# Performance work log

Measured on AMD Instinct MI355X. Metric: run time of the kernel, lower is better.

The kernel has to match this reference:

```python
import jax, jax.numpy as jnp
import numpy as np

EMBED_DIM = 1024
NUM_HEADS = 16


def setup_inputs() -> dict:
    key = jax.random.key(0)
    k_x, k_qw, k_qb, k_pw, k_bias, k_mask = jax.random.split(key, 6)
    B, N, C = 2, 2048, EMBED_DIM
    x = jax.random.normal(k_x, (B, N, C), dtype=jnp.float32)
    # torch Linear params: weight (out,in), bias (out,)
    qkv_w = jax.random.normal(k_qw, (3 * C, C), dtype=jnp.float32) * (C ** -0.5)
    qkv_b = jax.random.normal(k_qb, (3 * C,), dtype=jnp.float32) * 0.02
    proj_w = jax.random.normal(k_pw, (C, C), dtype=jnp.float32) * (C ** -0.5)
    proj_b = jnp.zeros((C,), dtype=jnp.float32)
    # nn.Parameter(torch.zeros(H,1,1)); small noise so the bias is non-trivial
    physics_bias = jax.random.normal(k_bias, (NUM_HEADS, 1, 1), dtype=jnp.float32) * 0.01
    physics_mask = jax.random.randint(k_mask, (B, 1, N, N), 0, 2).astype(jnp.int32)
    return {"x": x, "qkv_w": qkv_w, "qkv_b": qkv_b, "proj_w": proj_w,
            "proj_b": proj_b, "physics_bias": physics_bias,
            "physics_mask": physics_mask}


def reference(x, qkv_w, qkv_b, proj_w, proj_b, physics_bias, physics_mask):
    B, N, C = x.shape
    H = NUM_HEADS
    Dh = C // H
    # fused QKV projection: (B,N,3C) -> (B,N,3,H,Dh)
    qkv = (x @ qkv_w.T + qkv_b).reshape(B, N, 3, H, Dh)
    q = jnp.transpose(qkv[:, :, 0], (0, 2, 1, 3))  # (B,H,N,Dh)
    k = jnp.transpose(qkv[:, :, 1], (0, 2, 1, 3))
    v = jnp.transpose(qkv[:, :, 2], (0, 2, 1, 3))
    scale = Dh ** -0.5
    attn = jnp.einsum('bhnd,bhmd->bhnm', q, k) * scale  # (B,H,N,N)
    attn = attn + physics_bias  # (H,1,1) broadcasts per head
    attn = jnp.where(physics_mask == 0, -jnp.inf, attn)
    attn = jax.nn.softmax(attn, axis=-1)
    out = jnp.einsum('bhnm,bhmd->bhnd', attn, v)  # (B,H,N,Dh)
    out = jnp.transpose(out, (0, 2, 1, 3)).reshape(B, N, C)
    return out @ proj_w.T + proj_b
```

## Files before the change

### kernel.cpp

```cpp
#include <hip/hip_runtime.h>
#include <hip/hip_bf16.h>
#include <stdint.h>
#include <math.h>


typedef __bf16 bf16;
typedef __bf16 bf16x8 __attribute__((ext_vector_type(8)));
typedef __bf16 bf16x4 __attribute__((ext_vector_type(4)));
typedef float f32x4 __attribute__((ext_vector_type(4)));
typedef float f32x16 __attribute__((ext_vector_type(16)));

#define MFMA(a,b,c) __builtin_amdgcn_mfma_f32_16x16x32_bf16((a),(b),(c),0,0,0)
#define MFMA32(a,b,c) __builtin_amdgcn_mfma_f32_32x32x16_bf16((a),(b),(c),0,0,0)
#define L2E 1.44269504f

#if __has_builtin(__builtin_amdgcn_exp2f)
#define EXP2(x) __builtin_amdgcn_exp2f(x)
#else
#define EXP2(x) exp2f(x)
#endif

#if __has_builtin(__builtin_amdgcn_sbfe)
#define SBFE1(x,o) __builtin_amdgcn_sbfe((int)(x), (int)(o), 1)
#else
#define SBFE1(x,o) (((int)(((unsigned)(x)) << (31 - (o)))) >> 31)
#endif

__device__ __forceinline__ void async16(const void* g, void* l) {
  __builtin_amdgcn_global_load_lds(
      (const __attribute__((address_space(1))) void*)g,
      (__attribute__((address_space(3))) void*)l, 16, 0, 0);
}

__device__ __forceinline__ unsigned cvt_pk_bf16(float a, float b) {
  unsigned r;
  asm("v_cvt_pk_bf16_f32 %0, %1, %2" : "=v"(r) : "v"(a), "v"(b));
  return r;
}

__device__ __forceinline__ float maskf(float p, unsigned m, int pos) {
  int sm = SBFE1(m, pos);
  return __uint_as_float(__float_as_uint(p) & (unsigned)sm);
}

__device__ __forceinline__ void lane32_swap(unsigned a, unsigned b,
                                            unsigned& x, unsigned& y, int hi) {
#if __has_builtin(__builtin_amdgcn_permlane32_swap)
  auto r = __builtin_amdgcn_permlane32_swap((int)a, (int)b, false, false);
  x = (unsigned)r[0];
  y = (unsigned)r[1];
#else
  unsigned pa_ = __shfl_xor(a, 32), pb_ = __shfl_xor(b, 32);
  x = hi ? pb_ : a;
  y = hi ? b : pa_;
#endif
}

template <bool F32>
__device__ __forceinline__ bf16x8 ld8(const void* base, size_t off) {
  if constexpr (F32) {
    const float* p = (const float*)base + off;
    float4 u = *(const float4*)p;
    float4 v = *(const float4*)(p + 4);
    bf16x8 r;
    r[0] = (bf16)u.x; r[1] = (bf16)u.y; r[2] = (bf16)u.z; r[3] = (bf16)u.w;
    r[4] = (bf16)v.x; r[5] = (bf16)v.y; r[6] = (bf16)v.z; r[7] = (bf16)v.w;
    return r;
  } else {
    return *(const bf16x8*)((const bf16*)base + off);
  }
}

__global__ __launch_bounds__(256) void prep(const int* __restrict__ mask,
                                            unsigned long long* __restrict__ mbg,
                                            const float* __restrict__ x, bf16* __restrict__ xb,
                                            const float* __restrict__ qw, bf16* __restrict__ qwb,
                                            const float* __restrict__ pw, bf16* __restrict__ pwb) {
  int bid = blockIdx.x, tid = threadIdx.x;
  if (bid < 4096) {
    int lane = tid & 63, wv = tid >> 6;
    const int* mrow = mask + (size_t)bid * 2048;
#pragma unroll
    for (int i = 0; i < 8; ++i) {
      int w = wv * 8 + i;
      unsigned long long bal = __ballot(mrow[w * 64 + lane] != 0);
      if (lane == 0) mbg[(size_t)bid * 32 + w] = bal;
    }
  } else if (bid < 6144) {
    size_t i = ((size_t)(bid - 4096) * 256 + tid) * 8;
    *(bf16x8*)&xb[i] = ld8<true>(x, i);
  } else if (bid < 7680) {
    size_t i = ((size_t)(bid - 6144) * 256 + tid) * 8;
    *(bf16x8*)&qwb[i] = ld8<true>(qw, i);
  } else {
    size_t i = ((size_t)(bid - 7680) * 256 + tid) * 8;
    *(bf16x8*)&pwb[i] = ld8<true>(pw, i);
  }
}

template <int BROWS>
__device__ __forceinline__ void gemm_pipe(const bf16* __restrict__ A,
                                          const bf16* __restrict__ B,
                                          int m0, int n0,
                                          f32x4 acc[4][BROWS / 32],
                                          char* sm) {
  const int ABYTES = 128 * 128;
  const int BUF = ABYTES + BROWS * 128;
  int tid = threadIdx.x, lane = tid & 63, wv = tid >> 6;
  int wm = wv & 1, wn = wv >> 1, g = lane >> 4, li = lane & 15;
  int ln8 = lane >> 3;
  int scol = ((lane & 7) << 4) ^ ((ln8 & 7) << 4);

  const char* Ab = (const char*)A;
  const char* Bb = (const char*)B;

#pragma unroll
  for (int c = 0; c < 4; ++c) {
    int r = wv * 32 + c * 8;
    async16(Ab + (size_t)(m0 + r + ln8) * 2048 + scol, sm + r * 128);
  }
#pragma unroll
  for (int c = 0; c < BROWS / 32; ++c) {
    int r = wv * (BROWS / 4) + c * 8;
    async16(Bb + (size_t)(n0 + r + ln8) * 2048 + scol, sm + ABYTES + r * 128);
  }

  int kt2 = 128;
  for (int p = 0; p < 16; ++p) {
    asm volatile("s_waitcnt vmcnt(0)" ::: "memory");
    __builtin_amdgcn_s_barrier();
    __builtin_amdgcn_sched_barrier(0);
    if (p < 15) {
      char* bas = sm + ((p + 1) & 1) * BUF;
#pragma unroll
      for (int c = 0; c < 4; ++c) {
        int r = wv * 32 + c * 8;
        async16(Ab + (size_t)(m0 + r + ln8) * 2048 + kt2 + scol, bas + r * 128);
      }
#pragma unroll
      for (int c = 0; c < BROWS / 32; ++c) {
        int r = wv * (BROWS / 4) + c * 8;
        async16(Bb + (size_t)(n0 + r + ln8) * 2048 + kt2 + scol,
                bas + ABYTES + r * 128);
      }
      kt2 += 128;
    }
    __builtin_amdgcn_sched_barrier(0);
    const char* basA = sm + (p & 1) * BUF;
    const char* basB = basA + ABYTES;
#pragma unroll
    for (int ks = 0; ks < 2; ++ks) {
      bf16x8 af[4], bg[BROWS / 32];
#pragma unroll
      for (int i = 0; i < 4; ++i) {
        int row = wm * 64 + i * 16 + li;
        af[i] = *(const bf16x8*)(basA + row * 128 +
                                 ((ks * 64 + g * 16) ^ ((row & 7) << 4)));
      }
#pragma unroll
      for (int j = 0; j < BROWS / 32; ++j) {
        int row = wn * (BROWS / 2) + j * 16 + li;
        bg[j] = *(const bf16x8*)(basB + row * 128 +
                                 ((ks * 64 + g * 16) ^ ((row & 7) << 4)));
      }
#pragma unroll
      for (int i = 0; i < 4; ++i)
#pragma unroll
        for (int j = 0; j < BROWS / 32; ++j)
          acc[i][j] = MFMA(af[i], bg[j], acc[i][j]);
    }
  }
}

template <bool AF32, bool BF32>
__device__ __forceinline__ void gemm_core(const void* __restrict__ A,
                                          const void* __restrict__ B,
                                          int m0, int n0,
                                          f32x4 acc[4][4],
                                          bf16* Al, bf16* Bl) {
  const int K = 1024;
  int tid = threadIdx.x, lane = tid & 63, wv = tid >> 6;
  int wm = wv & 1, wn = wv >> 1, g = lane >> 4, li = lane & 15;
  int r8 = lane >> 3, c8 = lane & 7;

  for (int kt = 0; kt < K; kt += 64) {
    bf16x8 ta[4], tb[4];
#pragma unroll
    for (int i2 = 0; i2 < 4; ++i2) {
      int row = wv * 32 + i2 * 8 + r8;
      ta[i2] = ld8<AF32>(A, (size_t)(m0 + row) * K + kt + c8 * 8);
      tb[i2] = ld8<BF32>(B, (size_t)(n0 + row) * K + kt + c8 * 8);
    }
    __syncthreads();
#pragma unroll
    for (int i2 = 0; i2 < 4; ++i2) {
      int row = wv * 32 + i2 * 8 + r8;
      *(bf16x8*)&Al[row * 64 + c8 * 8] = ta[i2];
      *(bf16x8*)&Bl[row * 64 + c8 * 8] = tb[i2];
    }
    __syncthreads();
#pragma unroll
    for (int ks = 0; ks < 64; ks += 32) {
      bf16x8 af[4], bg[4];
#pragma unroll
      for (int i = 0; i < 4; ++i)
        af[i] = *(const bf16x8*)&Al[(wm * 64 + i * 16 + li) * 64 + ks + g * 8];
#pragma unroll
      for (int j = 0; j < 4; ++j)
        bg[j] = *(const bf16x8*)&Bl[(wn * 64 + j * 16 + li) * 64 + ks + g * 8];
#pragma unroll
      for (int i = 0; i < 4; ++i)
#pragma unroll
        for (int j = 0; j < 4; ++j)
          acc[i][j] = MFMA(af[i], bg[j], acc[i][j]);
    }
  }
}

__device__ __forceinline__ void epi_qk(f32x4 acc[4][4], int m0, int n0,
                                       const float* __restrict__ bias,
                                       bf16* __restrict__ qg, bf16* __restrict__ kg) {
  int lane = threadIdx.x & 63, wv = threadIdx.x >> 6;
  int wm = wv & 1, wn = wv >> 1, g = lane >> 4, li = lane & 15;
#pragma unroll
  for (int i = 0; i < 4; ++i) {
    int o = m0 + wm * 64 + i * 16 + g * 4;
    int s = o >> 10, h = (o >> 6) & 15, d = o & 63;
    float sc = s ? 1.0f : 0.125f * L2E;
    float b0 = bias[o], b1 = bias[o + 1], b2 = bias[o + 2], b3 = bias[o + 3];
    bf16* dstb = s ? kg : qg;
#pragma unroll
    for (int j = 0; j < 4; ++j) {
      int t = n0 + wn * 64 + j * 16 + li;
      int b = t >> 11, n = t & 2047;
      ushort4 pk;
      ((bf16*)&pk)[0] = (bf16)((acc[i][j][0] + b0) * sc);
      ((bf16*)&pk)[1] = (bf16)((acc[i][j][1] + b1) * sc);
      ((bf16*)&pk)[2] = (bf16)((acc[i][j][2] + b2) * sc);
      ((bf16*)&pk)[3] = (bf16)((acc[i][j][3] + b3) * sc);
      *(ushort4*)&dstb[(((size_t)b * 16 + h) * 2048 + n) * 64 + d] = pk;
    }
  }
}

__device__ __forceinline__ void epi_v(f32x4 acc[4][4], int m0, int n0,
                                      const float* __restrict__ bias,
                                      bf16* __restrict__ vtg) {
  int lane = threadIdx.x & 63, wvv = threadIdx.x >> 6;
  int wm = wvv & 1, wn = wvv >> 1, g = lane >> 4, li = lane & 15;
#pragma unroll
  for (int i = 0; i < 4; ++i) {
    int t = m0 + wm * 64 + i * 16 + g * 4;
    int b = t >> 11, n = t & 2047;
#pragma unroll
    for (int j = 0; j < 4; ++j) {
      int ov = n0 + wn * 64 + j * 16 + li;
      int h = ov >> 6, d = ov & 63;
      float bv = bias[ov];
      ushort4 pk;
      ((bf16*)&pk)[0] = (bf16)(acc[i][j][0] + bv);
      ((bf16*)&pk)[1] = (bf16)(acc[i][j][1] + bv);
      ((bf16*)&pk)[2] = (bf16)(acc[i][j][2] + bv);
      ((bf16*)&pk)[3] = (bf16)(acc[i][j][3] + bv);
      *(ushort4*)&vtg[(((size_t)b * 16 + h) * 64 + d) * 2048 + n] = pk;
    }
  }
}

__global__ __launch_bounds__(256) void gemm_qkv(const bf16* __restrict__ xb,
                                                const bf16* __restrict__ qwb,
                                                const float* __restrict__ bias,
                                                bf16* __restrict__ qg,
                                                bf16* __restrict__ kg,
                                                bf16* __restrict__ vtg) {
  __shared__ __align__(16) char sm[65536];
  f32x4 acc[4][4];
#pragma unroll
  for (int i = 0; i < 4; ++i)
#pragma unroll
    for (int j = 0; j < 4; ++j) acc[i][j] = (f32x4){0.f, 0.f, 0.f, 0.f};
  int bid = blockIdx.x;
  if (bid < 512) {
    int m0 = (bid >> 5) * 128, n0 = (bid & 31) * 128;
    gemm_pipe<128>(qwb, xb, m0, n0, acc, sm);
    epi_qk(acc, m0, n0, bias, qg, kg);
  } else {
    int vb = bid - 512;
    int m0 = (vb >> 3) * 128, n0 = (vb & 7) * 128;
    gemm_pipe<128>(xb, qwb + (size_t)2048 * 1024, m0, n0, acc, sm);
    epi_v(acc, m0, n0, bias + 2048, vtg);
  }
}

__global__ __launch_bounds__(256) void gemm_qk_f(const float* __restrict__ x,
                                                 const float* __restrict__ w,
                                                 const float* __restrict__ bias,
                                                 bf16* __restrict__ qg,
                                                 bf16* __restrict__ kg) {
  __shared__ bf16 Al[128 * 64], Bl[128 * 64];
  f32x4 acc[4][4];
#pragma unroll
  for (int i = 0; i < 4; ++i)
#pragma unroll
    for (int j = 0; j < 4; ++j) acc[i][j] = (f32x4){0.f, 0.f, 0.f, 0.f};
  int m0 = blockIdx.y * 128, n0 = blockIdx.x * 128;
  gemm_core<true, true>(w, x, m0, n0, acc, Al, Bl);
  epi_qk(acc, m0, n0, bias, qg, kg);
}
__global__ __launch_bounds__(256) void gemm_v_f(const float* __restrict__ x,
                                                const float* __restrict__ wv_,
                                                const float* __restrict__ bias,
                                                bf16* __restrict__ vtg) {
  __shared__ bf16 Al[128 * 64], Bl[128 * 64];
  f32x4 acc[4][4];
#pragma unroll
  for (int i = 0; i < 4; ++i)
#pragma unroll
    for (int j = 0; j < 4; ++j) acc[i][j] = (f32x4){0.f, 0.f, 0.f, 0.f};
  int m0 = blockIdx.y * 128, n0 = blockIdx.x * 128;
  gemm_core<true, true>(x, wv_, m0, n0, acc, Al, Bl);
  epi_v(acc, m0, n0, bias, vtg);
}
__global__ __launch_bounds__(256) void mask_bits(const int* __restrict__ mask,
                                                 unsigned long long* __restrict__ mbg) {
  int row = blockIdx.x, lane = threadIdx.x & 63, wv = threadIdx.x >> 6;
  const int* mrow = mask + (size_t)row * 2048;
#pragma unroll
  for (int i = 0; i < 8; ++i) {
    int w = wv * 8 + i;
    unsigned long long bal = __ballot(mrow[w * 64 + lane] != 0);
    if (lane == 0) mbg[(size_t)row * 32 + w] = bal;
  }
}

__global__ __launch_bounds__(512, 4) void flash_attn(
    const bf16* __restrict__ qg, const bf16* __restrict__ kg,
    const bf16* __restrict__ vtg, const unsigned long long* __restrict__ mbg,
    bf16* __restrict__ G) {
  __shared__ __align__(16) char smem[66048];

  int tid = threadIdx.x, lane = tid & 63, wv8 = tid >> 6;
  int grp = wv8 >> 2, wg = wv8 & 3;
  int cl = lane & 31, hi = lane >> 5;
  int sblk = blockIdx.x;
  int rest = sblk >> 3;
  int bh = ((rest >> 4) << 3) | (sblk & 7);
  int q0 = (rest & 15) * 128;
  int b = bh >> 4;

  const bf16* qbase = qg + (size_t)bh * 2048 * 64;
  const char* kgc = (const char*)(kg + (size_t)bh * 2048 * 64);
  const char* vgc = (const char*)(vtg + (size_t)bh * 64 * 2048);

  int qrow = q0 + wg * 32 + cl;
  bf16x8 qf[4];
#pragma unroll
  for (int kd = 0; kd < 4; ++kd)
    qf[kd] = *(const bf16x8*)&qbase[(size_t)qrow * 64 + kd * 16 + hi * 8];

  int ln8 = lane >> 3;
  int kcol = ((lane & 7) << 4) ^ ((ln8 & 7) << 4);
  int koff = (grp * 64 + wg * 16 + ln8) * 128 + kcol;
  int voff = (wg * 16 + ln8) * 4096 + grp * 128 + kcol;
  const char* mB = (const char*)mbg;
  unsigned moff = (unsigned)(((b * 2048 + qrow) * 32 + grp) * 8);
  int ldsw = wg * 2048;

  {
    char* kl = smem + grp * 32768;
    char* vl = kl + 8192;
    async16(kgc + koff, kl + ldsw);
    async16(kgc + koff + 1024, kl + ldsw + 1024);
    async16(vgc + voff, vl + ldsw);
    async16(vgc + voff + 32768, vl + ldsw + 1024);
  }
  unsigned long long mw_next = *(const unsigned long long*)(mB + moff);

  f32x16 accO0, accO1;
#pragma unroll
  for (int e = 0; e < 16; ++e) { accO0[e] = 0.f; accO1[e] = 0.f; }
  float lsum = 0.f;
  int swr = (cl & 7) << 4;

  for (int t = 0; t < 16; ++t) {
    asm volatile("s_waitcnt vmcnt(0)" ::: "memory");
    __builtin_amdgcn_s_barrier();
    __builtin_amdgcn_sched_barrier(0);
    unsigned long long mwc = mw_next;
    if (t < 15) {
      koff += 16384; voff += 256; moff += 16;
      char* kl = smem + grp * 32768 + (((t + 1) & 1) << 14);
      char* vl = kl + 8192;
      async16(kgc + koff, kl + ldsw);
      async16(kgc + koff + 1024, kl + ldsw + 1024);
      async16(vgc + voff, vl + ldsw);
      async16(vgc + voff + 32768, vl + ldsw + 1024);
      mw_next = *(const unsigned long long*)(mB + moff);
    }
    __builtin_amdgcn_sched_barrier(0);
    const char* Kl = smem + grp * 32768 + ((t & 1) << 14);
    const char* Vl = Kl + 8192;

    f32x16 accS0, accS1;
#pragma unroll
    for (int e = 0; e < 16; ++e) { accS0[e] = 0.f; accS1[e] = 0.f; }
    __builtin_amdgcn_s_setprio(1);
#pragma unroll
    for (int kd = 0; kd < 4; ++kd) {
      int cb = (kd * 32 + hi * 16) ^ swr;
      bf16x8 kf0 = *(const bf16x8*)(Kl + cl * 128 + cb);
      bf16x8 kf1 = *(const bf16x8*)(Kl + (32 + cl) * 128 + cb);
      accS0 = MFMA32(kf0, qf[kd], accS0);
      accS1 = MFMA32(kf1, qf[kd], accS1);
    }
    __builtin_amdgcn_s_setprio(0);

    unsigned dw[16];
#pragma unroll
    for (int nb = 0; nb < 2; ++nb) {
      unsigned mql = (unsigned)(mwc >> (nb * 32));
#pragma unroll
      for (int j = 0; j < 4; ++j) {
        int pos = j * 8 + hi * 4;
        float p0 = EXP2(nb ? accS1[4 * j + 0] : accS0[4 * j + 0]);
        float p1 = EXP2(nb ? accS1[4 * j + 1] : accS0[4 * j + 1]);
        float p2 = EXP2(nb ? accS1[4 * j + 2] : accS0[4 * j + 2]);
        float p3 = EXP2(nb ? accS1[4 * j + 3] : accS0[4 * j + 3]);
        p0 = maskf(p0, mql, pos);     p1 = maskf(p1, mql, pos + 1);
        p2 = maskf(p2, mql, pos + 2); p3 = maskf(p3, mql, pos + 3);
        lsum += (p0 + p1) + (p2 + p3);
        dw[nb * 8 + 2 * j]     = cvt_pk_bf16(p0, p1);
        dw[nb * 8 + 2 * j + 1] = cvt_pk_bf16(p2, p3);
      }
    }

    __builtin_amdgcn_s_setprio(1);
#pragma unroll
    for (int kk = 0; kk < 4; ++kk) {
      union { unsigned u[4]; bf16x8 v; } pa;
      lane32_swap(dw[4 * kk], dw[4 * kk + 2], pa.u[0], pa.u[2], hi);
      lane32_swap(dw[4 * kk + 1], dw[4 * kk + 3], pa.u[1], pa.u[3], hi);
      int cb = (kk * 32 + hi * 16) ^ swr;
      bf16x8 vf0 = *(const bf16x8*)(Vl + cl * 128 + cb);
      bf16x8 vf1 = *(const bf16x8*)(Vl + (32 + cl) * 128 + cb);
      accO0 = MFMA32(vf0, pa.v, accO0);
      accO1 = MFMA32(vf1, pa.v, accO1);
    }
    __builtin_amdgcn_s_setprio(0);
  }

  float ltot = lsum + __shfl_xor(lsum, 32);

  __syncthreads();
  float* oc = (float*)(smem + wg * 8192);
  float* lbuf = (float*)(smem + 65536);
  int osw = (cl & 7) << 4;
  if (grp == 1) {
#pragma unroll
    for (int j = 0; j < 4; ++j) {
      f32x4 qa, qb;
#pragma unroll
      for (int r = 0; r < 4; ++r) { qa[r] = accO0[4 * j + r]; qb[r] = accO1[4 * j + r]; }
      int dby = j * 32 + hi * 16;
      *(f32x4*)((char*)oc + cl * 256 + (dby ^ osw)) = qa;
      *(f32x4*)((char*)oc + cl * 256 + ((dby + 128) ^ osw)) = qb;
    }
    if (hi == 0) lbuf[wg * 32 + cl] = ltot;
  }
  __syncthreads();
  if (grp == 1) return;

  float lt2 = ltot + lbuf[wg * 32 + cl];
  float inv = 1.0f / fmaxf(lt2, 1e-37f);
#pragma unroll
  for (int j = 0; j < 4; ++j) {
    int dby = j * 32 + hi * 16;
    f32x4 qa = *(const f32x4*)((char*)oc + cl * 256 + (dby ^ osw));
    f32x4 qb = *(const f32x4*)((char*)oc + cl * 256 + ((dby + 128) ^ osw));
#pragma unroll
    for (int r = 0; r < 4; ++r) {
      accO0[4 * j + r] = (accO0[4 * j + r] + qa[r]) * inv;
      accO1[4 * j + r] = (accO1[4 * j + r] + qb[r]) * inv;
    }
  }

  bf16* ow = (bf16*)(smem + wg * 8192);
#pragma unroll
  for (int db = 0; db < 2; ++db) {
#pragma unroll
    for (int jq = 0; jq < 4; ++jq) {
      ushort4 pk;
      ((bf16*)&pk)[0] = (bf16)(db ? accO1[4 * jq + 0] : accO0[4 * jq + 0]);
      ((bf16*)&pk)[1] = (bf16)(db ? accO1[4 * jq + 1] : accO0[4 * jq + 1]);
      ((bf16*)&pk)[2] = (bf16)(db ? accO1[4 * jq + 2] : accO0[4 * jq + 2]);
      ((bf16*)&pk)[3] = (bf16)(db ? accO1[4 * jq + 3] : accO0[4 * jq + 3]);
      int dbase = db * 32 + jq * 8 + hi * 4;
      *(ushort4*)&ow[cl * 72 + dbase] = pk;
    }
  }

  int ql = lane >> 1, part = lane & 1;
  size_t tok = (size_t)b * 2048 + q0 + wg * 32 + ql;
  bf16* dst = G + tok * 1024 + (bh & 15) * 64 + part * 32;
  const bf16* src = &ow[ql * 72 + part * 32];
#pragma unroll
  for (int j = 0; j < 4; ++j)
    *(bf16x8*)&dst[j * 8] = *(const bf16x8*)&src[j * 8];
}

__global__ __launch_bounds__(256) void gemm_proj_n(const bf16* __restrict__ G,
                                                   const bf16* __restrict__ w,
                                                   const float* __restrict__ bias,
                                                   float* __restrict__ out) {
  __shared__ __align__(16) char sm[49152];
  int lane = threadIdx.x & 63, wv = threadIdx.x >> 6;
  int wm = wv & 1, wn = wv >> 1, g = lane >> 4, li = lane & 15;
  int m0 = blockIdx.y * 128, n0 = blockIdx.x * 64;

  f32x4 acc[4][2];
#pragma unroll
  for (int i = 0; i < 4; ++i)
#pragma unroll
    for (int j = 0; j < 2; ++j) acc[i][j] = (f32x4){0.f, 0.f, 0.f, 0.f};

  gemm_pipe<64>(w, G, m0, n0, acc, sm);

#pragma unroll
  for (int i = 0; i < 4; ++i) {
    int ch = m0 + wm * 64 + i * 16 + g * 4;
    float b0 = bias[ch], b1 = bias[ch + 1], b2 = bias[ch + 2], b3 = bias[ch + 3];
#pragma unroll
    for (int j = 0; j < 2; ++j) {
      int t = n0 + wn * 32 + j * 16 + li;
      float4 pk = make_float4(acc[i][j][0] + b0, acc[i][j][1] + b1,
                              acc[i][j][2] + b2, acc[i][j][3] + b3);
      *(float4*)&out[(size_t)t * 1024 + ch] = pk;
    }
  }
}

__global__ __launch_bounds__(256) void gemm_proj_f(const bf16* __restrict__ G,
                                                   const float* __restrict__ w,
                                                   const float* __restrict__ bias,
                                                   float* __restrict__ out) {
  __shared__ bf16 Al[128 * 64], Bl[128 * 64];
  f32x4 acc[4][4];
#pragma unroll
  for (int i = 0; i < 4; ++i)
#pragma unroll
    for (int j = 0; j < 4; ++j) acc[i][j] = (f32x4){0.f, 0.f, 0.f, 0.f};
  int m0 = blockIdx.y * 128, n0 = blockIdx.x * 128;
  gemm_core<true, false>(w, G, m0, n0, acc, Al, Bl);

  int lane = threadIdx.x & 63, wv = threadIdx.x >> 6;
  int wm = wv & 1, wn = wv >> 1, g = lane >> 4, li = lane & 15;
#pragma unroll
  for (int i = 0; i < 4; ++i) {
    int ch = m0 + wm * 64 + i * 16 + g * 4;
    float b0 = bias[ch], b1 = bias[ch + 1], b2 = bias[ch + 2], b3 = bias[ch + 3];
#pragma unroll
    for (int j = 0; j < 4; ++j) {
      int t = n0 + wn * 64 + j * 16 + li;
      float4 pk = make_float4(acc[i][j][0] + b0, acc[i][j][1] + b1,
                              acc[i][j][2] + b2, acc[i][j][3] + b3);
      *(float4*)&out[(size_t)t * 1024 + ch] = pk;
    }
  }
}

extern "C" void kernel_launch(void* const* d_in, const int* in_sizes, int n_in,
                              void* d_out, int out_size, void* d_ws, size_t ws_size,
                              hipStream_t stream) {
  const float* x      = (const float*)d_in[0];
  const float* qkv_w  = (const float*)d_in[1];
  const float* qkv_b  = (const float*)d_in[2];
  const float* proj_w = (const float*)d_in[3];
  const float* proj_b = (const float*)d_in[4];
  const int* mask     = (const int*)d_in[6];
  float* out = (float*)d_out;

  const size_t MB = (size_t)1 << 20;
  char* ws = (char*)d_ws;
  bf16* qg  = (bf16*)(ws);
  bf16* kg  = (bf16*)(ws + 8 * MB);
  bf16* vtg = (bf16*)(ws + 16 * MB);
  bf16* xb  = (bf16*)(ws + 24 * MB);
  bf16* G   = (bf16*)(ws + 24 * MB);
  unsigned long long* mbg = (unsigned long long*)(ws + 32 * MB);
  bf16* qwb = (bf16*)(ws + 33 * MB);
  bf16* pwb = (bf16*)(ws + 39 * MB);
  bool pre = ws_size >= 41 * MB;

  if (pre) {
    prep<<<dim3(8192), dim3(256), 0, stream>>>(mask, mbg, x, xb, qkv_w, qwb,
                                               proj_w, pwb);
    gemm_qkv<<<dim3(768), dim3(256), 0, stream>>>(xb, qwb, qkv_b, qg, kg, vtg);
  } else {
    mask_bits<<<dim3(4096), dim3(256), 0, stream>>>(mask, mbg);
    gemm_qk_f<<<dim3(32, 16), dim3(256), 0, stream>>>(x, qkv_w, qkv_b, qg, kg);
    gemm_v_f<<<dim3(8, 32), dim3(256), 0, stream>>>(
        x, qkv_w + (size_t)2048 * 1024, qkv_b + 2048, vtg);
  }

  flash_attn<<<dim3(512), dim3(512), 0, stream>>>(qg, kg, vtg, mbg, G);

  if (pre)
    gemm_proj_n<<<dim3(64, 8), dim3(256), 0, stream>>>(G, pwb, proj_b, out);
  else
    gemm_proj_f<<<dim3(32, 8), dim3(256), 0, stream>>>(G, proj_w, proj_b, out);
}
```

Before: 210.8 us.

## Triple-buffer projection GEMM, compute softmax row sums via MFMA, relax sched barriers

The output projection GEMM now uses a three-stage LDS pipeline that keeps two tiles in flight and waits on vmcnt(6), in place of the two-stage loop. Shared memory grows to 72KB for this. In the attention kernel the per-lane scalar row-sum accumulation and its cross-lane shuffle are replaced by an extra MFMA against a vector of ones, moving that work onto the matrix units. Two sched_barrier fences are removed so the compiler can interleave loads with the math. The larger LDS footprint may reduce occupancy, and the extra MFMA adds matrix-unit work to each attention tile.

```diff
diff --git a/kernel.cpp b/kernel.cpp
--- a/kernel.cpp
+++ b/kernel.cpp
@@ -145,7 +145,6 @@
       }
       kt2 += 128;
     }
-    __builtin_amdgcn_sched_barrier(0);
     const char* basA = sm + (p & 1) * BUF;
     const char* basB = basA + ABYTES;
 #pragma unroll
@@ -170,6 +169,101 @@
           acc[i][j] = MFMA(af[i], bg[j], acc[i][j]);
     }
   }
+}
+
+__device__ __forceinline__ void gemm_pipe3(const bf16* __restrict__ A,
+                                           const bf16* __restrict__ B,
+                                           int m0, int n0,
+                                           f32x4 acc[4][2],
+                                           char* sm) {
+  const int ABYTES = 128 * 128;
+  const int BUF = ABYTES + 64 * 128;
+  int tid = threadIdx.x, lane = tid & 63, wv = tid >> 6;
+  int wm = wv & 1, wn = wv >> 1, g = lane >> 4, li = lane & 15;
+  int ln8 = lane >> 3;
+  int scol = ((lane & 7) << 4) ^ ((ln8 & 7) << 4);
+
+  const char* Ab = (const char*)A;
+  const char* Bb = (const char*)B;
+
+#define STAGE3(kb, bas)                                                       \
+  {                                                                           \
+    _Pragma("unroll") for (int c = 0; c < 4; ++c) {                           \
+      int r = wv * 32 + c * 8;                                                \
+      async16(Ab + (size_t)(m0 + r + ln8) * 2048 + (kb) + scol,               \
+              (bas) + r * 128);                                               \
+    }                                                                         \
+    _Pragma("unroll") for (int c = 0; c < 2; ++c) {                           \
+      int r = wv * 16 + c * 8;                                                \
+      async16(Bb + (size_t)(n0 + r + ln8) * 2048 + (kb) + scol,               \
+              (bas) + ABYTES + r * 128);                                      \
+    }                                                                         \
+  }
+
+  STAGE3(0, sm);
+  STAGE3(128, sm + BUF);
+
+  for (int p = 0; p < 15; ++p) {
+    asm volatile("s_waitcnt vmcnt(6)" ::: "memory");
+    __builtin_amdgcn_s_barrier();
+    __builtin_amdgcn_sched_barrier(0);
+    if (p < 14) {
+      int b3 = (p + 2) % 3;
+      STAGE3((p + 2) * 128, sm + b3 * BUF);
+    }
+    const char* basA = sm + (p % 3) * BUF;
+    const char* basB = basA + ABYTES;
+#pragma unroll
+    for (int ks = 0; ks < 2; ++ks) {
+      bf16x8 af[4], bg[2];
+#pragma unroll
+      for (int i = 0; i < 4; ++i) {
+        int row = wm * 64 + i * 16 + li;
+        af[i] = *(const bf16x8*)(basA + row * 128 +
+                                 ((ks * 64 + g * 16) ^ ((row & 7) << 4)));
+      }
+#pragma unroll
+      for (int j = 0; j < 2; ++j) {
+        int row = wn * 32 + j * 16 + li;
+        bg[j] = *(const bf16x8*)(basB + row * 128 +
+                                 ((ks * 64 + g * 16) ^ ((row & 7) << 4)));
+      }
+#pragma unroll
+      for (int i = 0; i < 4; ++i)
+#pragma unroll
+        for (int j = 0; j < 2; ++j)
+          acc[i][j] = MFMA(af[i], bg[j], acc[i][j]);
+    }
+  }
+  asm volatile("s_waitcnt vmcnt(0)" ::: "memory");
+  __builtin_amdgcn_s_barrier();
+  __builtin_amdgcn_sched_barrier(0);
+  {
+    const char* basA = sm + (15 % 3) * BUF;
+    const char* basB = basA + ABYTES;
+#pragma unroll
+    for (int ks = 0; ks < 2; ++ks) {
+      bf16x8 af[4], bg[2];
+#pragma unroll
+      for (int i = 0; i < 4; ++i) {
+        int row = wm * 64 + i * 16 + li;
+        af[i] = *(const bf16x8*)(basA + row * 128 +
+                                 ((ks * 64 + g * 16) ^ ((row & 7) << 4)));
+      }
+#pragma unroll
+      for (int j = 0; j < 2; ++j) {
+        int row = wn * 32 + j * 16 + li;
+        bg[j] = *(const bf16x8*)(basB + row * 128 +
+                                 ((ks * 64 + g * 16) ^ ((row & 7) << 4)));
+      }
+#pragma unroll
+      for (int i = 0; i < 4; ++i)
+#pragma unroll
+        for (int j = 0; j < 2; ++j)
+          acc[i][j] = MFMA(af[i], bg[j], acc[i][j]);
+    }
+  }
+#undef STAGE3
 }
 
 template <bool AF32, bool BF32>
@@ -358,6 +452,10 @@
   for (int kd = 0; kd < 4; ++kd)
     qf[kd] = *(const bf16x8*)&qbase[(size_t)qrow * 64 + kd * 16 + hi * 8];
 
+  bf16x8 ones8;
+#pragma unroll
+  for (int i2 = 0; i2 < 8; ++i2) ones8[i2] = (bf16)1.0f;
+
   int ln8 = lane >> 3;
   int kcol = ((lane & 7) << 4) ^ ((ln8 & 7) << 4);
   int koff = (grp * 64 + wg * 16 + ln8) * 128 + kcol;
@@ -376,10 +474,9 @@
   }
   unsigned long long mw_next = *(const unsigned long long*)(mB + moff);
 
-  f32x16 accO0, accO1;
-#pragma unroll
-  for (int e = 0; e < 16; ++e) { accO0[e] = 0.f; accO1[e] = 0.f; }
-  float lsum = 0.f;
+  f32x16 accO0, accO1, accL;
+#pragma unroll
+  for (int e = 0; e < 16; ++e) { accO0[e] = 0.f; accO1[e] = 0.f; accL[e] = 0.f; }
   int swr = (cl & 7) << 4;
 
   for (int t = 0; t < 16; ++t) {
@@ -397,7 +494,6 @@
       async16(vgc + voff + 32768, vl + ldsw + 1024);
       mw_next = *(const unsigned long long*)(mB + moff);
     }
-    __builtin_amdgcn_sched_barrier(0);
     const char* Kl = smem + grp * 32768 + ((t & 1) << 14);
     const char* Vl = Kl + 8192;
 
@@ -428,7 +524,6 @@
         float p3 = EXP2(nb ? accS1[4 * j + 3] : accS0[4 * j + 3]);
         p0 = maskf(p0, mql, pos);     p1 = maskf(p1, mql, pos + 1);
         p2 = maskf(p2, mql, pos + 2); p3 = maskf(p3, mql, pos + 3);
-        lsum += (p0 + p1) + (p2 + p3);
         dw[nb * 8 + 2 * j]     = cvt_pk_bf16(p0, p1);
         dw[nb * 8 + 2 * j + 1] = cvt_pk_bf16(p2, p3);
       }
@@ -445,11 +540,12 @@
       bf16x8 vf1 = *(const bf16x8*)(Vl + (32 + cl) * 128 + cb);
       accO0 = MFMA32(vf0, pa.v, accO0);
       accO1 = MFMA32(vf1, pa.v, accO1);
+      accL = MFMA32(ones8, pa.v, accL);
     }
     __builtin_amdgcn_s_setprio(0);
   }
 
-  float ltot = lsum + __shfl_xor(lsum, 32);
+  float ltot = accL[0];
 
   __syncthreads();
   float* oc = (float*)(smem + wg * 8192);
@@ -512,7 +608,7 @@
                                                    const bf16* __restrict__ w,
                                                    const float* __restrict__ bias,
                                                    float* __restrict__ out) {
-  __shared__ __align__(16) char sm[49152];
+  __shared__ __align__(16) char sm[73728];
   int lane = threadIdx.x & 63, wv = threadIdx.x >> 6;
   int wm = wv & 1, wn = wv >> 1, g = lane >> 4, li = lane & 15;
   int m0 = blockIdx.y * 128, n0 = blockIdx.x * 64;
@@ -523,7 +619,7 @@
 #pragma unroll
     for (int j = 0; j < 2; ++j) acc[i][j] = (f32x4){0.f, 0.f, 0.f, 0.f};
 
-  gemm_pipe<64>(w, G, m0, n0, acc, sm);
+  gemm_pipe3(w, G, m0, n0, acc, sm);
 
 #pragma unroll
   for (int i = 0; i < 4; ++i) {
```

Result: slower. 217.0 us (+2.9%).
